# Optimization experiments

Measured on AMD Instinct MI355X. Metric: run time of the kernel, lower is better.

The kernel has to match this reference:

```python
import jax, jax.numpy as jnp
import numpy as np

N_NODES = 10000
N_EDGES = 160000
N_MAP = 50000
F_DIM = 128
N_RBF = 20
CUTOFF = 5.0
NUM_CONV = 3
EPS = 1e-15


def _w(k, shape):
    # simple fan-in scaled init for Dense weights (stored as (L, in, out))
    return jax.random.normal(k, shape, jnp.float32) * (1.0 / float(np.sqrt(shape[-2])))


def setup_inputs() -> dict:
    key = jax.random.key(0)
    ks = jax.random.split(key, 16)
    cg_xyz = jax.random.normal(ks[0], (N_NODES, 3), jnp.float32)
    src = jax.random.randint(ks[1], (N_EDGES,), 0, N_NODES)
    off = jax.random.randint(ks[2], (N_EDGES,), 1, N_NODES)
    dst = (src + off) % N_NODES  # directed neighbor list, no self-edges
    CG_nbr_list = jnp.stack([src, dst], axis=-1)
    mapping = jax.random.randint(ks[3], (N_MAP,), 0, N_NODES)
    H = jax.random.normal(ks[4], (N_NODES, F_DIM), jnp.float32)
    L, F = NUM_CONV, F_DIM
    params = dict(
        msg_W1=_w(ks[5], (L, 2 * F, 2 * F)), msg_b1=jnp.zeros((L, 2 * F), jnp.float32),
        msg_W2=_w(ks[6], (L, 2 * F, 5 * F)), msg_b2=jnp.zeros((L, 5 * F), jnp.float32),
        dist_W=_w(ks[7], (L, N_RBF, 5 * F)), dist_b=jnp.zeros((L, 5 * F), jnp.float32),
        upd_U=_w(ks[8], (L, F, F)), upd_V=_w(ks[9], (L, F, F)),
        upd_W1=_w(ks[10], (L, 2 * F, F)), upd_b1=jnp.zeros((L, F), jnp.float32),
        upd_W2=_w(ks[11], (L, F, 3 * F)), upd_b2=jnp.zeros((L, 3 * F), jnp.float32),
    )
    return dict(cg_xyz=cg_xyz, CG_nbr_list=CG_nbr_list, mapping=mapping, H=H, **params)


def reference(cg_xyz, CG_nbr_list, mapping, H,
              msg_W1, msg_b1, msg_W2, msg_b2, dist_W, dist_b,
              upd_U, upd_V, upd_W1, upd_b1, upd_W2, upd_b2):
    act = jax.nn.silu  # 'swish'
    N = H.shape[0]
    src = CG_nbr_list[:, 0]
    dst = CG_nbr_list[:, 1]
    # edge geometry (preprocess_r)
    r_ij = cg_xyz[dst] - cg_xyz[src]                 # (E, 3)
    dist = jnp.sqrt(jnp.sum(r_ij ** 2, axis=-1))     # (E,)
    unit = r_ij / dist[:, None]                      # (E, 3)
    # PaiNN radial basis sin(n*pi*d/cutoff)/d and cosine cutoff envelope
    n = jnp.arange(1, N_RBF + 1, dtype=cg_xyz.dtype)
    rbf = jnp.sin(n[None, :] * (jnp.pi / CUTOFF) * dist[:, None]) / dist[:, None]  # (E, n_rbf)
    env = jnp.where(dist < CUTOFF, 0.5 * (jnp.cos(jnp.pi * dist / CUTOFF) + 1.0), 0.0)  # (E,)
    # state init (breaksym=False -> Sbar zeros)
    V = jnp.zeros((N, F_DIM, 3), H.dtype)
    Sbar = jnp.zeros_like(H)
    Vbar = jnp.zeros_like(V)
    for l in range(NUM_CONV):
        # ---- EquiMessagePsuedo ----
        s_cat = jnp.concatenate([H, Sbar], axis=-1)                          # (N, 2F)
        phi = act(s_cat @ msg_W1[l] + msg_b1[l]) @ msg_W2[l] + msg_b2[l]     # (N, 5F)
        w_s = (rbf @ dist_W[l] + dist_b[l]) * env[:, None]                   # (E, 5F)
        inv = (phi[dst] * w_s).reshape(-1, 5, F_DIM)                         # (E, 5, F)
        gate_v = inv[:, 0, :][..., None]   # gates v_j
        ds = inv[:, 1, :]
        dir_coef = inv[:, 2, :][..., None]  # scales unit vector (shared)
        dsbar = inv[:, 3, :]
        gate_vbar = inv[:, 4, :][..., None]  # gates vbar_j
        unit_add = dir_coef * unit[:, None, :]                               # (E, F, 3)
        dv_ij = unit_add + gate_v * V[dst]
        dvbar_ij = unit_add + gate_vbar * Vbar[dst]
        H = H + jax.ops.segment_sum(ds, src, num_segments=N)
        Sbar = Sbar + jax.ops.segment_sum(dsbar, src, num_segments=N)
        V = V + jax.ops.segment_sum(dv_ij, src, num_segments=N)
        Vbar = Vbar + jax.ops.segment_sum(dvbar_ij, src, num_segments=N)
        # ---- UpdateBlock (standard PaiNN update) ----
        u_v = jnp.einsum('nfd,fg->ngd', V, upd_U[l])                          # (N, F, 3)
        v_v = jnp.einsum('nfd,fg->ngd', V, upd_V[l])                          # (N, F, 3)
        v_norm = jnp.sqrt(jnp.sum(v_v ** 2, axis=-1) + EPS)                   # (N, F)
        s_stack = jnp.concatenate([H, v_norm], axis=-1)                       # (N, 2F)
        a = act(s_stack @ upd_W1[l] + upd_b1[l]) @ upd_W2[l] + upd_b2[l]      # (N, 3F)
        a = a.reshape(-1, 3, F_DIM)
        dV_u = u_v * a[:, 0, :][..., None]
        dH_u = a[:, 1, :] * jnp.sum(u_v * v_v, axis=-1) + a[:, 2, :]
        H = H + dH_u
        V = V + dV_u
    return H, V
```

## Files before the change

### kernel.cpp

```cpp
#include <hip/hip_runtime.h>
#include <math.h>

#define NN 10000
#define NE 160000
#define FDIM 128
#define NRBF 20
#define PI_F 3.14159265358979323846f
#define LDP 40

typedef short bf16x8 __attribute__((ext_vector_type(8)));
typedef float f32x4 __attribute__((ext_vector_type(4)));

__device__ __forceinline__ unsigned short f2bf_rne(float v) {
    unsigned int u = __float_as_uint(v);
    u += 0x7FFF + ((u >> 16) & 1);
    return (unsigned short)(u >> 16);
}
__device__ __forceinline__ float bf2f(unsigned short b) {
    return __uint_as_float(((unsigned int)b) << 16);
}

__global__ void edge_count_kernel(const int* __restrict__ nbr, int* __restrict__ counts)
{
    int e = blockIdx.x * blockDim.x + threadIdx.x;
    if (e >= NE) return;
    atomicAdd(&counts[nbr[2 * e]], 1);
}

__global__ void scan_kernel(const int* __restrict__ counts, int* __restrict__ offsets)
{
    __shared__ int sd[1024];
    __shared__ int carry;
    if (threadIdx.x == 0) carry = 0;
    __syncthreads();
    for (int base = 0; base < NN; base += 1024) {
        int i = base + threadIdx.x;
        int v = (i < NN) ? counts[i] : 0;
        sd[threadIdx.x] = v;
        __syncthreads();
        for (int off = 1; off < 1024; off <<= 1) {
            int t = (threadIdx.x >= off) ? sd[threadIdx.x - off] : 0;
            __syncthreads();
            sd[threadIdx.x] += t;
            __syncthreads();
        }
        if (i < NN) offsets[i] = carry + sd[threadIdx.x] - v;
        __syncthreads();
        if (threadIdx.x == 0) carry += sd[1023];
        __syncthreads();
    }
    if (threadIdx.x == 0) offsets[NN] = carry;
}

__global__ void edge_geom_fill_kernel(const float* __restrict__ xyz, const int* __restrict__ nbr,
                                      const int* __restrict__ offsets, int* __restrict__ cnt2,
                                      int* __restrict__ dstP, float4* __restrict__ ueP,
                                      float* __restrict__ rbfP)
{
    int e = blockIdx.x * blockDim.x + threadIdx.x;
    if (e >= NE) return;
    int s = nbr[2 * e], d = nbr[2 * e + 1];
    float dx = xyz[3 * d + 0] - xyz[3 * s + 0];
    float dy = xyz[3 * d + 1] - xyz[3 * s + 1];
    float dz = xyz[3 * d + 2] - xyz[3 * s + 2];
    float dist = sqrtf(dx * dx + dy * dy + dz * dz);
    float inv = 1.0f / dist;
    int p = offsets[s] + atomicAdd(&cnt2[s], 1);
    dstP[p] = d;
    const float c = PI_F / 5.0f;
    float env = (dist < 5.0f) ? 0.5f * (cosf(c * dist) + 1.0f) : 0.0f;
    ueP[p] = make_float4(dx * inv, dy * inv, dz * inv, env);
#pragma unroll
    for (int k = 0; k < NRBF; k++)
        rbfP[NRBF * p + k] = sinf((float)(k + 1) * c * dist) * inv;
}

template <int ACT, int CAT>
__global__ __launch_bounds__(256) void gemm3_kernel(
    const float* __restrict__ A0, const float* __restrict__ A1,
    const float* __restrict__ W, const float* __restrict__ bias,
    float* __restrict__ C, int M, int K, int N)
{
    __shared__ __align__(16) unsigned short Ah[64 * LDP];
    __shared__ __align__(16) unsigned short Al[64 * LDP];
    __shared__ __align__(16) unsigned short Bh[64 * LDP];
    __shared__ __align__(16) unsigned short Bl[64 * LDP];

    int tid = threadIdx.x;
    int row0 = blockIdx.y * 64, col0 = blockIdx.x * 64;
    int lane = tid & 63, wave = tid >> 6;
    int mb = (wave & 1) * 32, nb = (wave >> 1) * 32;
    int lm = lane & 15, quad = lane >> 4;

    f32x4 acc[2][2] = {};

    int ra = tid >> 2, kq = tid & 3;
    int kr = tid >> 3, nq = tid & 7;

    for (int k0 = 0; k0 < K; k0 += 32) {
        {
            int ar = row0 + ra;
            float4 a0 = make_float4(0.f, 0.f, 0.f, 0.f);
            float4 a1 = make_float4(0.f, 0.f, 0.f, 0.f);
            if (ar < M) {
                const float* Ab;
                if (CAT) Ab = (k0 < 128) ? A0 + (size_t)ar * 128 + k0
                                         : A1 + (size_t)ar * 128 + (k0 - 128);
                else     Ab = A0 + (size_t)ar * K + k0;
                a0 = *(const float4*)(Ab + kq * 4);
                a1 = *(const float4*)(Ab + kq * 4 + 16);
            }
            float v0[4] = {a0.x, a0.y, a0.z, a0.w};
            float v1[4] = {a1.x, a1.y, a1.z, a1.w};
            ushort4 h0, l0, h1, l1;
            unsigned short* hp0 = (unsigned short*)&h0;
            unsigned short* lp0 = (unsigned short*)&l0;
            unsigned short* hp1 = (unsigned short*)&h1;
            unsigned short* lp1 = (unsigned short*)&l1;
#pragma unroll
            for (int i = 0; i < 4; i++) {
                unsigned short h = f2bf_rne(v0[i]);
                hp0[i] = h; lp0[i] = f2bf_rne(v0[i] - bf2f(h));
                unsigned short g = f2bf_rne(v1[i]);
                hp1[i] = g; lp1[i] = f2bf_rne(v1[i] - bf2f(g));
            }
            *(ushort4*)&Ah[ra * LDP + kq * 4]      = h0;
            *(ushort4*)&Al[ra * LDP + kq * 4]      = l0;
            *(ushort4*)&Ah[ra * LDP + kq * 4 + 16] = h1;
            *(ushort4*)&Al[ra * LDP + kq * 4 + 16] = l1;
        }
        {
            const float* Wb = &W[(size_t)(k0 + kr) * N + col0];
            float4 b0 = *(const float4*)(Wb + nq * 4);
            float4 b1 = *(const float4*)(Wb + nq * 4 + 32);
            float v0[4] = {b0.x, b0.y, b0.z, b0.w};
            float v1[4] = {b1.x, b1.y, b1.z, b1.w};
#pragma unroll
            for (int i = 0; i < 4; i++) {
                int n = nq * 4 + i;
                unsigned short h = f2bf_rne(v0[i]);
                Bh[n * LDP + kr] = h;
                Bl[n * LDP + kr] = f2bf_rne(v0[i] - bf2f(h));
                int n2 = n + 32;
                unsigned short g = f2bf_rne(v1[i]);
                Bh[n2 * LDP + kr] = g;
                Bl[n2 * LDP + kr] = f2bf_rne(v1[i] - bf2f(g));
            }
        }
        __syncthreads();
        bf16x8 fah[2], fal[2], fbh[2], fbl[2];
#pragma unroll
        for (int mt = 0; mt < 2; mt++) {
            int r = mb + mt * 16 + lm;
            fah[mt] = *(const bf16x8*)&Ah[r * LDP + quad * 8];
            fal[mt] = *(const bf16x8*)&Al[r * LDP + quad * 8];
        }
#pragma unroll
        for (int nt = 0; nt < 2; nt++) {
            int n = nb + nt * 16 + lm;
            fbh[nt] = *(const bf16x8*)&Bh[n * LDP + quad * 8];
            fbl[nt] = *(const bf16x8*)&Bl[n * LDP + quad * 8];
        }
#pragma unroll
        for (int mt = 0; mt < 2; mt++)
#pragma unroll
            for (int nt = 0; nt < 2; nt++) {
                acc[mt][nt] = __builtin_amdgcn_mfma_f32_16x16x32_bf16(
                    fah[mt], fbh[nt], acc[mt][nt], 0, 0, 0);
                acc[mt][nt] = __builtin_amdgcn_mfma_f32_16x16x32_bf16(
                    fah[mt], fbl[nt], acc[mt][nt], 0, 0, 0);
                acc[mt][nt] = __builtin_amdgcn_mfma_f32_16x16x32_bf16(
                    fal[mt], fbh[nt], acc[mt][nt], 0, 0, 0);
            }
        __syncthreads();
    }
#pragma unroll
    for (int mt = 0; mt < 2; mt++)
#pragma unroll
        for (int nt = 0; nt < 2; nt++) {
            int c = col0 + nb + nt * 16 + lm;
            float bv = bias ? bias[c] : 0.f;
#pragma unroll
            for (int reg = 0; reg < 4; reg++) {
                int r = row0 + mb + mt * 16 + quad * 4 + reg;
                if (r >= M) continue;
                float v = acc[mt][nt][reg] + bv;
                if (ACT) v = v / (1.0f + expf(-v));
                C[(size_t)r * N + c] = v;
            }
        }
}

__global__ __launch_bounds__(256, 2) void gather_kernel(
    const int* __restrict__ offsets, const int* __restrict__ dstP,
    const float4* __restrict__ ueP, const float* __restrict__ rbfP,
    const float* __restrict__ phi,
    const float* __restrict__ distW, const float* __restrict__ distb,
    const float* __restrict__ Vold, const float* __restrict__ Vbold,
    float* __restrict__ H, float* __restrict__ Sbar,
    float* __restrict__ Vnew, float* __restrict__ Vbnew)
{
    int n = (blockIdx.x << 1) | (threadIdx.x >> 7);
    int f = threadIdx.x & 127;

    float wv[100];
#pragma unroll
    for (int k = 0; k < NRBF; k++)
#pragma unroll
        for (int c = 0; c < 5; c++)
            wv[k * 5 + c] = distW[k * 640 + c * 128 + f];
#pragma unroll
    for (int i = 0; i < 100; i++) asm volatile("" : "+v"(wv[i]));

    float b0 = distb[f], b1 = distb[128 + f], b2 = distb[256 + f],
          b3 = distb[384 + f], b4 = distb[512 + f];

    float accH = 0.f, accS = 0.f;
    float accV0 = 0.f, accV1 = 0.f, accV2 = 0.f;
    float accB0 = 0.f, accB1 = 0.f, accB2 = 0.f;
    int e0 = offsets[n], e1 = offsets[n + 1];
    for (int p = e0; p < e1; ++p) {
        int d = dstP[p];
        float4 ue = ueP[p];
        float r[NRBF];
#pragma unroll
        for (int q = 0; q < NRBF / 4; q++) {
            float4 rv = *(const float4*)&rbfP[NRBF * p + 4 * q];
            r[4 * q + 0] = rv.x; r[4 * q + 1] = rv.y;
            r[4 * q + 2] = rv.z; r[4 * q + 3] = rv.w;
        }
        float w0 = b0, w1 = b1, w2 = b2, w3 = b3, w4 = b4;
#pragma unroll
        for (int k = 0; k < NRBF; k++) {
            float rk = r[k];
            w0 += rk * wv[k * 5 + 0];
            w1 += rk * wv[k * 5 + 1];
            w2 += rk * wv[k * 5 + 2];
            w3 += rk * wv[k * 5 + 3];
            w4 += rk * wv[k * 5 + 4];
        }
        float ev = ue.w;
        const float* ph = phi + (size_t)d * 640;
        float i0 = ph[f] * w0 * ev;
        float i1 = ph[128 + f] * w1 * ev;
        float i2 = ph[256 + f] * w2 * ev;
        float i3 = ph[384 + f] * w3 * ev;
        float i4 = ph[512 + f] * w4 * ev;
        accH += i1;
        accS += i3;
        const float* vd  = Vold  + (size_t)d * 384;
        const float* vbd = Vbold + (size_t)d * 384;
        accV0 += i2 * ue.x + i0 * vd[f];
        accV1 += i2 * ue.y + i0 * vd[128 + f];
        accV2 += i2 * ue.z + i0 * vd[256 + f];
        accB0 += i2 * ue.x + i4 * vbd[f];
        accB1 += i2 * ue.y + i4 * vbd[128 + f];
        accB2 += i2 * ue.z + i4 * vbd[256 + f];
    }
    H[n * 128 + f] += accH;
    Sbar[n * 128 + f] += accS;
    const float* vo  = Vold  + (size_t)n * 384;
    const float* vbo = Vbold + (size_t)n * 384;
    float* vn  = Vnew  + (size_t)n * 384;
    float* vbn = Vbnew + (size_t)n * 384;
    vn[f]       = vo[f]       + accV0;
    vn[128 + f] = vo[128 + f] + accV1;
    vn[256 + f] = vo[256 + f] + accV2;
    vbn[f]       = vbo[f]       + accB0;
    vbn[128 + f] = vbo[128 + f] + accB1;
    vbn[256 + f] = vbo[256 + f] + accB2;
}

__global__ __launch_bounds__(128) void uv_kernel(const float* __restrict__ V,
                                                 const float* __restrict__ U,
                                                 const float* __restrict__ Vm,
                                                 float* __restrict__ u_v,
                                                 float* __restrict__ vnorm,
                                                 float* __restrict__ dotb)
{
    int g = threadIdx.x;
    int n0 = blockIdx.x * 4;
    __shared__ float sV[4 * 384];
    for (int i = g; i < 4 * 384; i += 128) {
        int nn = i / 384, rem = i % 384;
        int node = n0 + nn;
        sV[i] = (node < NN) ? V[(size_t)node * 384 + rem] : 0.f;
    }
    __syncthreads();
    float ua[4][3] = {}, va[4][3] = {};
    for (int ff = 0; ff < 128; ++ff) {
        float uf = U[ff * 128 + g];
        float vf = Vm[ff * 128 + g];
#pragma unroll
        for (int nn = 0; nn < 4; nn++) {
            float v0 = sV[nn * 384 + ff];
            float v1 = sV[nn * 384 + 128 + ff];
            float v2 = sV[nn * 384 + 256 + ff];
            ua[nn][0] += v0 * uf; ua[nn][1] += v1 * uf; ua[nn][2] += v2 * uf;
            va[nn][0] += v0 * vf; va[nn][1] += v1 * vf; va[nn][2] += v2 * vf;
        }
    }
#pragma unroll
    for (int nn = 0; nn < 4; nn++) {
        int node = n0 + nn;
        if (node >= NN) continue;
        float d = ua[nn][0] * va[nn][0] + ua[nn][1] * va[nn][1] + ua[nn][2] * va[nn][2];
        float vn = sqrtf(va[nn][0] * va[nn][0] + va[nn][1] * va[nn][1] +
                         va[nn][2] * va[nn][2] + 1e-15f);
        u_v[(size_t)node * 384 + g]       = ua[nn][0];
        u_v[(size_t)node * 384 + 128 + g] = ua[nn][1];
        u_v[(size_t)node * 384 + 256 + g] = ua[nn][2];
        vnorm[node * 128 + g] = vn;
        dotb[node * 128 + g] = d;
    }
}

template <int LAST>
__global__ void final_update_kernel(const float* __restrict__ a,
                                    const float* __restrict__ dotb,
                                    const float* __restrict__ u_v,
                                    float* __restrict__ H,
                                    float* __restrict__ Vplanar,
                                    float* __restrict__ Vout)
{
    int idx = blockIdx.x * blockDim.x + threadIdx.x;
    if (idx >= NN * 128) return;
    int n = idx >> 7, g = idx & 127;
    float a0 = a[n * 384 + g];
    float a1 = a[n * 384 + 128 + g];
    float a2 = a[n * 384 + 256 + g];
    H[idx] += a1 * dotb[idx] + a2;
    float* vp = Vplanar + (size_t)n * 384;
    const float* up = u_v + (size_t)n * 384;
    float v0 = vp[g]       + a0 * up[g];
    float v1 = vp[128 + g] + a0 * up[128 + g];
    float v2 = vp[256 + g] + a0 * up[256 + g];
    if (LAST) {
        float* o = Vout + (size_t)n * 384 + g * 3;
        o[0] = v0; o[1] = v1; o[2] = v2;
    } else {
        vp[g] = v0; vp[128 + g] = v1; vp[256 + g] = v2;
    }
}

extern "C" void kernel_launch(void* const* d_in, const int* in_sizes, int n_in,
                              void* d_out, int out_size, void* d_ws, size_t ws_size,
                              hipStream_t stream)
{
    const float* xyz    = (const float*)d_in[0];
    const int*   nbr    = (const int*)d_in[1];
    const float* H_in   = (const float*)d_in[3];
    const float* msgW1  = (const float*)d_in[4];
    const float* msgb1  = (const float*)d_in[5];
    const float* msgW2  = (const float*)d_in[6];
    const float* msgb2  = (const float*)d_in[7];
    const float* distW  = (const float*)d_in[8];
    const float* distb  = (const float*)d_in[9];
    const float* updU   = (const float*)d_in[10];
    const float* updV   = (const float*)d_in[11];
    const float* updW1  = (const float*)d_in[12];
    const float* updb1  = (const float*)d_in[13];
    const float* updW2  = (const float*)d_in[14];
    const float* updb2  = (const float*)d_in[15];

    float* out  = (float*)d_out;
    float* H    = out;
    float* Vout = out + NN * 128;

    float* f = (float*)d_ws;
    float* Va   = f; f += NN * 384;
    float* Vb   = f; f += NN * 384;
    float* Vba  = f; f += NN * 384;
    float* Vbb  = f; f += NN * 384;
    float* Sbar = f; f += NN * 128;
    float* X1   = f; f += NN * 256;
    float* phi  = f; f += NN * 640;
    float* u_v  = f; f += NN * 384;
    float4* ueP = (float4*)f; f += NE * 4;
    float* rbfP  = f; f += NE * NRBF;
    int* ip = (int*)f;
    int* counts  = ip; ip += NN;
    int* offsets = ip; ip += NN + 1;
    int* cnt2    = ip; ip += NN;
    int* dstP    = ip; ip += NE;
    float* vnorm = phi;
    float* dotb  = phi + NN * 128;
    float* abuf  = phi + NN * 256;

    hipMemsetAsync(counts, 0, NN * sizeof(int), stream);
    hipMemsetAsync(cnt2, 0, NN * sizeof(int), stream);
    hipMemsetAsync(Va, 0, (size_t)NN * 384 * sizeof(float), stream);
    hipMemsetAsync(Vba, 0, (size_t)NN * 384 * sizeof(float), stream);
    hipMemsetAsync(Sbar, 0, (size_t)NN * 128 * sizeof(float), stream);
    hipMemcpyAsync(H, H_in, (size_t)NN * 128 * sizeof(float),
                   hipMemcpyDeviceToDevice, stream);

    edge_count_kernel<<<(NE + 255) / 256, 256, 0, stream>>>(nbr, counts);
    scan_kernel<<<1, 1024, 0, stream>>>(counts, offsets);
    edge_geom_fill_kernel<<<(NE + 255) / 256, 256, 0, stream>>>(xyz, nbr, offsets, cnt2,
                                                                dstP, ueP, rbfP);

    for (int l = 0; l < 3; ++l) {
        const float* W1 = msgW1 + (size_t)l * 256 * 256;
        const float* b1 = msgb1 + (size_t)l * 256;
        const float* W2 = msgW2 + (size_t)l * 256 * 640;
        const float* b2 = msgb2 + (size_t)l * 640;
        const float* dW = distW + (size_t)l * NRBF * 640;
        const float* db = distb + (size_t)l * 640;
        const float* Ul = updU + (size_t)l * 128 * 128;
        const float* Vl = updV + (size_t)l * 128 * 128;
        const float* uW1 = updW1 + (size_t)l * 256 * 128;
        const float* ub1 = updb1 + (size_t)l * 128;
        const float* uW2 = updW2 + (size_t)l * 128 * 384;
        const float* ub2 = updb2 + (size_t)l * 384;

        float *Vold, *Vnew, *Vbold, *Vbnew;
        if (l == 0)      { Vold = Va; Vnew = Vb; Vbold = Vba; Vbnew = Vbb; }
        else if (l == 1) { Vold = Vb; Vnew = Va; Vbold = Vbb; Vbnew = Vba; }
        else             { Vold = Va; Vnew = Vb; Vbold = Vba; Vbnew = Vbb; }

        {
            dim3 g(256 / 64, (NN + 63) / 64);
            gemm3_kernel<1, 1><<<g, 256, 0, stream>>>(H, Sbar, W1, b1, X1, NN, 256, 256);
        }
        {
            dim3 g(640 / 64, (NN + 63) / 64);
            gemm3_kernel<0, 0><<<g, 256, 0, stream>>>(X1, nullptr, W2, b2, phi, NN, 256, 640);
        }

        gather_kernel<<<NN / 2, 256, 0, stream>>>(offsets, dstP, ueP, rbfP,
                                                  phi, dW, db, Vold, Vbold,
                                                  H, Sbar, Vnew, Vbnew);

        uv_kernel<<<(NN + 3) / 4, 128, 0, stream>>>(Vnew, Ul, Vl, u_v, vnorm, dotb);

        {
            dim3 g(128 / 64, (NN + 63) / 64);
            gemm3_kernel<1, 1><<<g, 256, 0, stream>>>(H, vnorm, uW1, ub1, X1, NN, 256, 128);
        }
        {
            dim3 g(384 / 64, (NN + 63) / 64);
            gemm3_kernel<0, 0><<<g, 256, 0, stream>>>(X1, nullptr, uW2, ub2, abuf, NN, 128, 384);
        }

        if (l < 2)
            final_update_kernel<0><<<(NN * 128 + 255) / 256, 256, 0, stream>>>(
                abuf, dotb, u_v, H, Vnew, nullptr);
        else
            final_update_kernel<1><<<(NN * 128 + 255) / 256, 256, 0, stream>>>(
                abuf, dotb, u_v, H, Vnew, Vout);
    }
}
```

Before: 1.030 ms.

## Split gather per node across halves and run U/V projection as matrix-core GEMM

The gather kernel now gives each node a full 256-thread block, with one half handling the V path and the other the Vbar path. This cuts the per-thread weight registers from 100 to 60 and raises the occupancy bound. The scalar uv_kernel is replaced by concatenating U and V into a 128x256 weight, running the existing bf16-split MFMA GEMM over the 3N planar V rows, and computing norm and dot in a small elementwise kernel. This adds a weight-concatenation kernel, a larger uv2 buffer and one extra launch per layer. Phi and the dst indices are now loaded by both halves.

```diff
diff --git a/kernel.cpp b/kernel.cpp
--- a/kernel.cpp
+++ b/kernel.cpp
@@ -73,6 +73,19 @@
 #pragma unroll
     for (int k = 0; k < NRBF; k++)
         rbfP[NRBF * p + k] = sinf((float)(k + 1) * c * dist) * inv;
+}
+
+__global__ void build_uvcat_kernel(const float* __restrict__ updU,
+                                   const float* __restrict__ updV,
+                                   float* __restrict__ UVcat)
+{
+    int idx = blockIdx.x * blockDim.x + threadIdx.x;
+    if (idx >= 3 * 128 * 256) return;
+    int l = idx / (128 * 256);
+    int rem = idx % (128 * 256);
+    int k = rem >> 8, j = rem & 255;
+    UVcat[idx] = (j < 128) ? updU[(l * 128 + k) * 128 + j]
+                           : updV[(l * 128 + k) * 128 + (j - 128)];
 }
 
 template <int ACT, int CAT>
@@ -191,7 +204,7 @@
         }
 }
 
-__global__ __launch_bounds__(256, 2) void gather_kernel(
+__global__ __launch_bounds__(256, 4) void gather_kernel(
     const int* __restrict__ offsets, const int* __restrict__ dstP,
     const float4* __restrict__ ueP, const float* __restrict__ rbfP,
     const float* __restrict__ phi,
@@ -200,24 +213,26 @@
     float* __restrict__ H, float* __restrict__ Sbar,
     float* __restrict__ Vnew, float* __restrict__ Vbnew)
 {
-    int n = (blockIdx.x << 1) | (threadIdx.x >> 7);
-    int f = threadIdx.x & 127;
-
-    float wv[100];
+    int n = blockIdx.x;
+    int t = threadIdx.x;
+    int half = t >> 7;
+    int f = t & 127;
+    int po = half * 256;
+
+    float wv[60];
 #pragma unroll
     for (int k = 0; k < NRBF; k++)
 #pragma unroll
-        for (int c = 0; c < 5; c++)
-            wv[k * 5 + c] = distW[k * 640 + c * 128 + f];
-#pragma unroll
-    for (int i = 0; i < 100; i++) asm volatile("" : "+v"(wv[i]));
-
-    float b0 = distb[f], b1 = distb[128 + f], b2 = distb[256 + f],
-          b3 = distb[384 + f], b4 = distb[512 + f];
-
-    float accH = 0.f, accS = 0.f;
-    float accV0 = 0.f, accV1 = 0.f, accV2 = 0.f;
-    float accB0 = 0.f, accB1 = 0.f, accB2 = 0.f;
+        for (int c = 0; c < 3; c++)
+            wv[k * 3 + c] = distW[k * 640 + po + c * 128 + f];
+#pragma unroll
+    for (int i = 0; i < 60; i++) asm volatile("" : "+v"(wv[i]));
+
+    float bA = distb[po + f], bB = distb[po + 128 + f], bC = distb[po + 256 + f];
+
+    const float* Vsel = half ? Vbold : Vold;
+
+    float sacc = 0.f, acc0 = 0.f, acc1 = 0.f, acc2 = 0.f;
     int e0 = offsets[n], e1 = offsets[n + 1];
     for (int p = e0; p < e1; ++p) {
         int d = dstP[p];
@@ -229,96 +244,53 @@
             r[4 * q + 0] = rv.x; r[4 * q + 1] = rv.y;
             r[4 * q + 2] = rv.z; r[4 * q + 3] = rv.w;
         }
-        float w0 = b0, w1 = b1, w2 = b2, w3 = b3, w4 = b4;
+        float wA = bA, wB = bB, wC = bC;
 #pragma unroll
         for (int k = 0; k < NRBF; k++) {
             float rk = r[k];
-            w0 += rk * wv[k * 5 + 0];
-            w1 += rk * wv[k * 5 + 1];
-            w2 += rk * wv[k * 5 + 2];
-            w3 += rk * wv[k * 5 + 3];
-            w4 += rk * wv[k * 5 + 4];
+            wA += rk * wv[k * 3 + 0];
+            wB += rk * wv[k * 3 + 1];
+            wC += rk * wv[k * 3 + 2];
         }
         float ev = ue.w;
-        const float* ph = phi + (size_t)d * 640;
-        float i0 = ph[f] * w0 * ev;
-        float i1 = ph[128 + f] * w1 * ev;
-        float i2 = ph[256 + f] * w2 * ev;
-        float i3 = ph[384 + f] * w3 * ev;
-        float i4 = ph[512 + f] * w4 * ev;
-        accH += i1;
-        accS += i3;
-        const float* vd  = Vold  + (size_t)d * 384;
-        const float* vbd = Vbold + (size_t)d * 384;
-        accV0 += i2 * ue.x + i0 * vd[f];
-        accV1 += i2 * ue.y + i0 * vd[128 + f];
-        accV2 += i2 * ue.z + i0 * vd[256 + f];
-        accB0 += i2 * ue.x + i4 * vbd[f];
-        accB1 += i2 * ue.y + i4 * vbd[128 + f];
-        accB2 += i2 * ue.z + i4 * vbd[256 + f];
+        const float* ph = phi + (size_t)d * 640 + po;
+        float iA = ph[f] * wA * ev;
+        float iB = ph[128 + f] * wB * ev;
+        float iC = ph[256 + f] * wC * ev;
+        float dir  = half ? iA : iC;
+        float gate = half ? iC : iA;
+        sacc += iB;
+        const float* vd = Vsel + (size_t)d * 384;
+        acc0 += dir * ue.x + gate * vd[f];
+        acc1 += dir * ue.y + gate * vd[128 + f];
+        acc2 += dir * ue.z + gate * vd[256 + f];
     }
-    H[n * 128 + f] += accH;
-    Sbar[n * 128 + f] += accS;
-    const float* vo  = Vold  + (size_t)n * 384;
-    const float* vbo = Vbold + (size_t)n * 384;
-    float* vn  = Vnew  + (size_t)n * 384;
-    float* vbn = Vbnew + (size_t)n * 384;
-    vn[f]       = vo[f]       + accV0;
-    vn[128 + f] = vo[128 + f] + accV1;
-    vn[256 + f] = vo[256 + f] + accV2;
-    vbn[f]       = vbo[f]       + accB0;
-    vbn[128 + f] = vbo[128 + f] + accB1;
-    vbn[256 + f] = vbo[256 + f] + accB2;
-}
-
-__global__ __launch_bounds__(128) void uv_kernel(const float* __restrict__ V,
-                                                 const float* __restrict__ U,
-                                                 const float* __restrict__ Vm,
-                                                 float* __restrict__ u_v,
-                                                 float* __restrict__ vnorm,
-                                                 float* __restrict__ dotb)
-{
-    int g = threadIdx.x;
-    int n0 = blockIdx.x * 4;
-    __shared__ float sV[4 * 384];
-    for (int i = g; i < 4 * 384; i += 128) {
-        int nn = i / 384, rem = i % 384;
-        int node = n0 + nn;
-        sV[i] = (node < NN) ? V[(size_t)node * 384 + rem] : 0.f;
-    }
-    __syncthreads();
-    float ua[4][3] = {}, va[4][3] = {};
-    for (int ff = 0; ff < 128; ++ff) {
-        float uf = U[ff * 128 + g];
-        float vf = Vm[ff * 128 + g];
-#pragma unroll
-        for (int nn = 0; nn < 4; nn++) {
-            float v0 = sV[nn * 384 + ff];
-            float v1 = sV[nn * 384 + 128 + ff];
-            float v2 = sV[nn * 384 + 256 + ff];
-            ua[nn][0] += v0 * uf; ua[nn][1] += v1 * uf; ua[nn][2] += v2 * uf;
-            va[nn][0] += v0 * vf; va[nn][1] += v1 * vf; va[nn][2] += v2 * vf;
-        }
-    }
-#pragma unroll
-    for (int nn = 0; nn < 4; nn++) {
-        int node = n0 + nn;
-        if (node >= NN) continue;
-        float d = ua[nn][0] * va[nn][0] + ua[nn][1] * va[nn][1] + ua[nn][2] * va[nn][2];
-        float vn = sqrtf(va[nn][0] * va[nn][0] + va[nn][1] * va[nn][1] +
-                         va[nn][2] * va[nn][2] + 1e-15f);
-        u_v[(size_t)node * 384 + g]       = ua[nn][0];
-        u_v[(size_t)node * 384 + 128 + g] = ua[nn][1];
-        u_v[(size_t)node * 384 + 256 + g] = ua[nn][2];
-        vnorm[node * 128 + g] = vn;
-        dotb[node * 128 + g] = d;
-    }
+    if (half == 0) H[n * 128 + f] += sacc;
+    else           Sbar[n * 128 + f] += sacc;
+    const float* vo = Vsel + (size_t)n * 384;
+    float* vn = (half ? Vbnew : Vnew) + (size_t)n * 384;
+    vn[f]       = vo[f]       + acc0;
+    vn[128 + f] = vo[128 + f] + acc1;
+    vn[256 + f] = vo[256 + f] + acc2;
+}
+
+__global__ void norm_kernel(const float* __restrict__ uv2,
+                            float* __restrict__ vnorm, float* __restrict__ dotb)
+{
+    int idx = blockIdx.x * blockDim.x + threadIdx.x;
+    if (idx >= NN * 128) return;
+    int n = idx >> 7, g = idx & 127;
+    const float* base = uv2 + (size_t)n * 768;
+    float u0 = base[g],       u1 = base[256 + g], u2 = base[512 + g];
+    float v0 = base[128 + g], v1 = base[384 + g], v2 = base[640 + g];
+    dotb[idx] = u0 * v0 + u1 * v1 + u2 * v2;
+    vnorm[idx] = sqrtf(v0 * v0 + v1 * v1 + v2 * v2 + 1e-15f);
 }
 
 template <int LAST>
 __global__ void final_update_kernel(const float* __restrict__ a,
                                     const float* __restrict__ dotb,
-                                    const float* __restrict__ u_v,
+                                    const float* __restrict__ uv2,
                                     float* __restrict__ H,
                                     float* __restrict__ Vplanar,
                                     float* __restrict__ Vout)
@@ -331,10 +303,10 @@
     float a2 = a[n * 384 + 256 + g];
     H[idx] += a1 * dotb[idx] + a2;
     float* vp = Vplanar + (size_t)n * 384;
-    const float* up = u_v + (size_t)n * 384;
-    float v0 = vp[g]       + a0 * up[g];
-    float v1 = vp[128 + g] + a0 * up[128 + g];
-    float v2 = vp[256 + g] + a0 * up[256 + g];
+    const float* ub = uv2 + (size_t)n * 768;
+    float v0 = vp[g]       + a0 * ub[g];
+    float v1 = vp[128 + g] + a0 * ub[256 + g];
+    float v2 = vp[256 + g] + a0 * ub[512 + g];
     if (LAST) {
         float* o = Vout + (size_t)n * 384 + g * 3;
         o[0] = v0; o[1] = v1; o[2] = v2;
@@ -375,7 +347,8 @@
     float* Sbar = f; f += NN * 128;
     float* X1   = f; f += NN * 256;
     float* phi  = f; f += NN * 640;
-    float* u_v  = f; f += NN * 384;
+    float* uv2  = f; f += NN * 768;
+    float* UVcat = f; f += 3 * 128 * 256;
     float4* ueP = (float4*)f; f += NE * 4;
     float* rbfP  = f; f += NE * NRBF;
     int* ip = (int*)f;
@@ -399,6 +372,7 @@
     scan_kernel<<<1, 1024, 0, stream>>>(counts, offsets);
     edge_geom_fill_kernel<<<(NE + 255) / 256, 256, 0, stream>>>(xyz, nbr, offsets, cnt2,
                                                                 dstP, ueP, rbfP);
+    build_uvcat_kernel<<<(3 * 128 * 256 + 255) / 256, 256, 0, stream>>>(updU, updV, UVcat);
 
     for (int l = 0; l < 3; ++l) {
         const float* W1 = msgW1 + (size_t)l * 256 * 256;
@@ -407,8 +381,7 @@
         const float* b2 = msgb2 + (size_t)l * 640;
         const float* dW = distW + (size_t)l * NRBF * 640;
         const float* db = distb + (size_t)l * 640;
-        const float* Ul = updU + (size_t)l * 128 * 128;
-        const float* Vl = updV + (size_t)l * 128 * 128;
+        const float* UVl = UVcat + (size_t)l * 128 * 256;
         const float* uW1 = updW1 + (size_t)l * 256 * 128;
         const float* ub1 = updb1 + (size_t)l * 128;
         const float* uW2 = updW2 + (size_t)l * 128 * 384;
@@ -428,11 +401,16 @@
             gemm3_kernel<0, 0><<<g, 256, 0, stream>>>(X1, nullptr, W2, b2, phi, NN, 256, 640);
         }
 
-        gather_kernel<<<NN / 2, 256, 0, stream>>>(offsets, dstP, ueP, rbfP,
-                                                  phi, dW, db, Vold, Vbold,
-                                                  H, Sbar, Vnew, Vbnew);
-
-        uv_kernel<<<(NN + 3) / 4, 128, 0, stream>>>(Vnew, Ul, Vl, u_v, vnorm, dotb);
+        gather_kernel<<<NN, 256, 0, stream>>>(offsets, dstP, ueP, rbfP,
+                                              phi, dW, db, Vold, Vbold,
+                                              H, Sbar, Vnew, Vbnew);
+
+        {
+            dim3 g(256 / 64, (3 * NN + 63) / 64);
+            gemm3_kernel<0, 0><<<g, 256, 0, stream>>>(Vnew, nullptr, UVl, nullptr,
+                                                      uv2, 3 * NN, 128, 256);
+        }
+        norm_kernel<<<(NN * 128 + 255) / 256, 256, 0, stream>>>(uv2, vnorm, dotb);
 
         {
             dim3 g(128 / 64, (NN + 63) / 64);
@@ -445,9 +423,9 @@
 
         if (l < 2)
             final_update_kernel<0><<<(NN * 128 + 255) / 256, 256, 0, stream>>>(
-                abuf, dotb, u_v, H, Vnew, nullptr);
+                abuf, dotb, uv2, H, Vnew, nullptr);
         else
             final_update_kernel<1><<<(NN * 128 + 255) / 256, 256, 0, stream>>>(
-                abuf, dotb, u_v, H, Vnew, Vout);
+                abuf, dotb, uv2, H, Vnew, Vout);
     }
 }
```

Measured after the change: 932.3 us. 9.5% less time.
